# Performance work log

Measured on AMD Instinct MI355X. Metric: run time of the kernel, lower is better.

## Reference

```python
import jax, jax.numpy as jnp
import numpy as np

B, M, E, H = 256, 196, 1024, 8
Dh = E // H          # 128 = att_mid_dim[0]
MID = 64             # att_mid_dim[1]
ALPHA = 1.3          # CELU alpha
EPS = 1e-5


def group_norm(x, w, b, groups=H, eps=EPS):
    # x: [N, C]; torch GroupNorm over channel groups
    N, C = x.shape
    xg = x.reshape(N, groups, C // groups)
    mu = xg.mean(-1, keepdims=True)
    var = xg.var(-1, keepdims=True)
    xn = ((xg - mu) * jax.lax.rsqrt(var + eps)).reshape(N, C)
    return xn * w + b


def proj(x, W, b, gw, gb):
    # Linear -> CELU(1.3) -> GroupNorm(H)
    return group_norm(jax.nn.celu(x @ W + b, alpha=ALPHA), gw, gb)


def setup_inputs() -> dict:
    key0 = jax.random.key(0)
    ks = jax.random.split(key0, 16)
    d = {}
    d["query"] = jax.random.normal(ks[0], (B, E), jnp.float32)
    d["key"] = jax.random.normal(ks[1], (B, M, E), jnp.float32)
    d["mask"] = jax.random.randint(ks[2], (B, M), 0, 2, jnp.int32)
    d["value1"] = jax.random.normal(ks[3], (B, E), jnp.float32)
    d["value2"] = jax.random.normal(ks[4], (B, M, E), jnp.float32)
    s = 0.02
    for i, nm in enumerate(["q", "k", "v1", "v2"]):
        d[f"W{nm}"] = jax.random.normal(ks[5 + i], (E, E), jnp.float32) * s
        d[f"b{nm}"] = jnp.zeros((E,), jnp.float32)
        d[f"g{nm}_w"] = jnp.ones((E,), jnp.float32)
        d[f"g{nm}_b"] = jnp.zeros((E,), jnp.float32)
    d["Wb"] = jax.random.normal(ks[9], (Dh, MID), jnp.float32) * s
    d["bb"] = jnp.zeros((MID,), jnp.float32)
    d["Ws"] = jax.random.normal(ks[10], (MID, 1), jnp.float32) * s
    d["bs"] = jnp.zeros((1,), jnp.float32)
    d["Wc"] = jax.random.normal(ks[11], (MID, Dh), jnp.float32) * s
    d["bc"] = jnp.zeros((Dh,), jnp.float32)
    return d


def reference(query, key, mask, value1, value2,
              Wq, bq, gq_w, gq_b, Wk, bk, gk_w, gk_b,
              Wv1, bv1, gv1_w, gv1_b, Wv2, bv2, gv2_w, gv2_b,
              Wb, bb, Ws, bs, Wc, bc):
    # input projections (dropout layers are identity at eval)
    q = proj(query, Wq, bq, gq_w, gq_b).reshape(B, H, Dh)
    v1 = proj(value1, Wv1, bv1, gv1_w, gv1_b).reshape(B, H, Dh)
    k = proj(key.reshape(-1, E), Wk, bk, gk_w, gk_b).reshape(B, M, H, Dh).transpose(0, 2, 1, 3)   # [B,H,M,Dh]
    v2 = proj(value2.reshape(-1, E), Wv2, bv2, gv2_w, gv2_b).reshape(B, M, H, Dh).transpose(0, 2, 1, 3)

    # SCAttDec
    att_map = q[:, :, None, :] * k                                # [B,H,M,Dh]
    hidden = jax.nn.relu(att_map @ Wb + bb)                       # [B,H,M,MID]
    maskf = mask.astype(hidden.dtype)                             # [B,M]
    mext = maskf[:, None, :, None]                                # [B,1,M,1]
    att_map_pool = jnp.sum(hidden * mext, axis=2) / jnp.sum(mext, axis=2)   # [B,H,MID]

    alpha_spatial = (hidden @ Ws + bs)[..., 0]                    # [B,H,M]
    alpha_spatial = jnp.where(mask[:, None, :] == 0, -1e9, alpha_spatial)
    alpha_spatial = jax.nn.softmax(alpha_spatial, axis=-1)
    v2_pooled = jnp.einsum("bhm,bhmd->bhd", alpha_spatial, v2)    # [B,H,Dh]

    alpha_channel = jax.nn.sigmoid(att_map_pool @ Wc + bc)        # [B,H,Dh]
    attn = v1 * v2_pooled * alpha_channel                         # [B,H,Dh]
    return attn.reshape(B, H * Dh)
```

## Files before the change

### kernel.cpp

```cpp
#include <hip/hip_runtime.h>

typedef unsigned short u16;
typedef unsigned int u32;
typedef unsigned long long u64;
typedef __attribute__((ext_vector_type(8))) short short8;
typedef __attribute__((ext_vector_type(4))) float floatx4;

#define E_ 1024
#define B_ 256
#define M_ 196
#define H_ 8
#define DH_ 128
#define MID_ 64
#define NKROW 50176

__device__ __forceinline__ u16 f2bf(float f){
  union { float f; u32 u; } v; v.f = f;
  return (u16)((v.u + (((v.u >> 16) & 1u) + 0x7fffu)) >> 16);
}
__device__ __forceinline__ float bf2f(u16 h){
  union { u32 u; float f; } v; v.u = ((u32)h) << 16;
  return v.f;
}
__device__ __forceinline__ u32 pack_bf2(float a, float b){
  u32 ua = __float_as_uint(a) + 0x8000u;
  u32 ub = __float_as_uint(b) + 0x8000u;
  return __builtin_amdgcn_perm(ub, ua, 0x07060302);
}
__device__ __forceinline__ void gl_lds16(const void* g, void* l){
  __builtin_amdgcn_global_load_lds(
      (const __attribute__((address_space(1))) u32*)g,
      (__attribute__((address_space(3))) u32*)l, 16, 0, 0);
}
__device__ __forceinline__ float celu_f(float x){
  float xn = 1.3f * (__expf(x * 0.76923076923f) - 1.0f);
  return x > 0.f ? x : xn;
}

__global__ __launch_bounds__(256) void xconv_kernel(
    float* __restrict__ key, float* __restrict__ value2,
    float* __restrict__ query, float* __restrict__ value1)
{
  int gr = blockIdx.x * 8 + (threadIdx.x >> 5);
  int i  = threadIdx.x & 31;
  float* X; int r;
  if (gr < NKROW)               { X = key;    r = gr; }
  else if (gr < 2*NKROW)        { X = value2; r = gr - NKROW; }
  else if (gr < 2*NKROW + B_)   { X = query;  r = gr - 2*NKROW; }
  else                          { X = value1; r = gr - 2*NKROW - B_; }
  const float4* src = (const float4*)(X + (size_t)r * E_);
  float4 v[8];
  #pragma unroll
  for (int j = 0; j < 8; j++) v[j] = src[j * 32 + i];
  __syncthreads();
  uint2* dst = (uint2*)((u16*)X + (size_t)r * 2048);
  #pragma unroll
  for (int j = 0; j < 8; j++){
    uint2 o;
    o.x = pack_bf2(v[j].x, v[j].y);
    o.y = pack_bf2(v[j].z, v[j].w);
    dst[j * 32 + i] = o;
  }
}

__global__ __launch_bounds__(256) void wconv_kernel(
    const float* __restrict__ Wq, const float* __restrict__ Wk,
    const float* __restrict__ Wv1, const float* __restrict__ Wv2,
    u16* __restrict__ Wt)
{
  __shared__ u16 tile[64][72];
  const float* W = (blockIdx.z == 0) ? Wq : (blockIdx.z == 1) ? Wk
                 : (blockIdx.z == 2) ? Wv1 : Wv2;
  u16* out = Wt + (size_t)blockIdx.z * (E_ * E_);
  int k0 = blockIdx.x * 64, c0 = blockIdx.y * 64;
  int tx = threadIdx.x & 63, ty = threadIdx.x >> 6;
  #pragma unroll
  for (int i = 0; i < 16; i++){
    int k = ty * 16 + i;
    tile[k][tx] = f2bf(W[(size_t)(k0 + k) * E_ + c0 + tx]);
  }
  __syncthreads();
  #pragma unroll
  for (int i = 0; i < 16; i++){
    int c = ty * 16 + i;
    out[(size_t)(c0 + c) * E_ + k0 + tx] = tile[tx][c];
  }
}

__global__ __launch_bounds__(512, 2) void proj_kernel(
    const u16* __restrict__ xq_, const u16* __restrict__ xk_,
    const u16* __restrict__ xv1_, const u16* __restrict__ xv2_,
    const float* __restrict__ bq, const float* __restrict__ gqw, const float* __restrict__ gqb,
    const float* __restrict__ bk, const float* __restrict__ gkw, const float* __restrict__ gkb,
    const float* __restrict__ bv1, const float* __restrict__ gv1w, const float* __restrict__ gv1b,
    const float* __restrict__ bv2, const float* __restrict__ gv2w, const float* __restrict__ gv2b,
    const u16* __restrict__ Wt,
    u16* __restrict__ qout, u16* __restrict__ khead,
    u16* __restrict__ v1out, u16* __restrict__ v2head)
{
  __shared__ __align__(16) u16 a_lds[2][256 * 32];
  __shared__ __align__(16) u16 b_lds[2][256 * 32];

  const int tid = threadIdx.x;
  const int w = tid >> 6, lane = tid & 63, qd = lane >> 4, lr = lane & 15;
  const int wm = w & 3, wn = w >> 2;

  const int mtb = blockIdx.x;
  const u16* X; const float *bias, *gw, *gb; u16* outp; int row0, matsel, hm;
  if (mtb < 196)      { X = xk_;  bias = bk;  gw = gkw;  gb = gkb;  outp = khead;  row0 = mtb*256;        matsel = 1; hm = 1; }
  else if (mtb < 392) { X = xv2_; bias = bv2; gw = gv2w; gb = gv2b; outp = v2head; row0 = (mtb-196)*256;  matsel = 3; hm = 1; }
  else if (mtb == 392){ X = xq_;  bias = bq;  gw = gqw;  gb = gqb;  outp = qout;   row0 = 0;              matsel = 0; hm = 0; }
  else                { X = xv1_; bias = bv1; gw = gv1w; gb = gv1b; outp = v1out;  row0 = 0;              matsel = 2; hm = 0; }
  const int cp = blockIdx.y, col0 = cp * 256;

  const int srow = lane >> 2, sslot = lane & 3, sswz = sslot ^ (srow & 3);
  const u16* aptr0 = X + (size_t)(row0 + (w*2    )*16 + srow) * 2048 + sswz * 8;
  const u16* aptr1 = X + (size_t)(row0 + (w*2 + 1)*16 + srow) * 2048 + sswz * 8;
  const u16* wbase = Wt + (size_t)matsel * (E_*E_);
  const u16* bptr0 = wbase + (size_t)(col0 + (w*2    )*16 + srow) * E_ + sswz * 8;
  const u16* bptr1 = wbase + (size_t)(col0 + (w*2 + 1)*16 + srow) * E_ + sswz * 8;

  floatx4 acc[4][8];
  #pragma unroll
  for (int i = 0; i < 4; i++)
    #pragma unroll
    for (int j = 0; j < 8; j++){
      floatx4 z = {0.f, 0.f, 0.f, 0.f};
      acc[i][j] = z;
    }

  gl_lds16(aptr0, &a_lds[0][(w*2    )*16*32]);
  gl_lds16(aptr1, &a_lds[0][(w*2 + 1)*16*32]);
  gl_lds16(bptr0, &b_lds[0][(w*2    )*16*32]);
  gl_lds16(bptr1, &b_lds[0][(w*2 + 1)*16*32]);
  __syncthreads();

  const int fslot = (qd ^ (lr & 3)) * 8;
  for (int kt = 0; kt < 32; kt++){
    const int cur = kt & 1, nxt = cur ^ 1;
    if (kt < 31){
      const int ko = (kt + 1) * 32;
      gl_lds16(aptr0 + ko, &a_lds[nxt][(w*2    )*16*32]);
      gl_lds16(aptr1 + ko, &a_lds[nxt][(w*2 + 1)*16*32]);
      gl_lds16(bptr0 + ko, &b_lds[nxt][(w*2    )*16*32]);
      gl_lds16(bptr1 + ko, &b_lds[nxt][(w*2 + 1)*16*32]);
    }
    short8 afr[4], bfr[8];
    #pragma unroll
    for (int m2 = 0; m2 < 4; m2++)
      afr[m2] = *(const short8*)&a_lds[cur][(wm*64 + m2*16 + lr)*32 + fslot];
    #pragma unroll
    for (int nt = 0; nt < 8; nt++)
      bfr[nt] = *(const short8*)&b_lds[cur][(wn*128 + nt*16 + lr)*32 + fslot];
    #pragma unroll
    for (int m2 = 0; m2 < 4; m2++)
      #pragma unroll
      for (int nt = 0; nt < 8; nt++)
        acc[m2][nt] = __builtin_amdgcn_mfma_f32_16x16x32_bf16(afr[m2], bfr[nt], acc[m2][nt], 0, 0, 0);
    __syncthreads();
  }

  float biasv[8], gwv[8], gbv[8];
  #pragma unroll
  for (int nt = 0; nt < 8; nt++){
    int c = col0 + wn*128 + nt*16 + lr;
    biasv[nt] = bias[c]; gwv[nt] = gw[c]; gbv[nt] = gb[c];
  }
  const int head = cp*2 + wn;
  #pragma unroll
  for (int m2 = 0; m2 < 4; m2++){
    #pragma unroll
    for (int r = 0; r < 4; r++){
      float s = 0.f, s2 = 0.f;
      #pragma unroll
      for (int nt = 0; nt < 8; nt++){
        float x = celu_f(acc[m2][nt][r] + biasv[nt]);
        acc[m2][nt][r] = x;
        s += x; s2 += x * x;
      }
      #pragma unroll
      for (int off = 1; off < 16; off <<= 1){
        s  += __shfl_xor(s,  off, 64);
        s2 += __shfl_xor(s2, off, 64);
      }
      float mean = s * 0.0078125f;
      float var  = s2 * 0.0078125f - mean * mean;
      float rstd = rsqrtf(var + 1e-5f);
      u32 rg = row0 + wm*64 + m2*16 + qd*4 + r;
      size_t base;
      if (hm){
        u32 bi = (u32)(((u64)rg * 171197ull) >> 25);
        u32 m  = rg - bi * 196u;
        base = ((size_t)(bi*H_ + head)*M_ + m) * DH_;
      } else {
        base = (size_t)rg * E_ + head * DH_;
      }
      #pragma unroll
      for (int nt = 0; nt < 8; nt++)
        outp[base + nt*16 + lr] = f2bf((acc[m2][nt][r] - mean) * rstd * gwv[nt] + gbv[nt]);
    }
  }
}

__global__ __launch_bounds__(256) void attn_kernel(
    const u16* __restrict__ qproj, const u16* __restrict__ khead,
    const u16* __restrict__ v1proj, const u16* __restrict__ v2head,
    const int* __restrict__ mask,
    const float* __restrict__ Wb, const float* __restrict__ bb,
    const float* __restrict__ Ws, const float* __restrict__ bs,
    const float* __restrict__ Wc, const float* __restrict__ bc,
    float* __restrict__ outp)
{
  __shared__ u16 wbt[64 * 136];
  __shared__ float qv[128];
  __shared__ float mrow[208];
  __shared__ float logitv[208];
  __shared__ float hsum_l[4][64];
  __shared__ float wexpv[208];
  __shared__ float poolv[64];
  __shared__ float v2acc[4][128];
  __shared__ float wc2[2][128];
  __shared__ float red[8];

  const int tid = threadIdx.x;
  const int w = tid >> 6, lane = tid & 63, qd = lane >> 4, lr = lane & 15;
  const int b = blockIdx.y, h = blockIdx.x;

  const u16* kbase  = khead  + (size_t)(b*H_ + h) * (M_*DH_);
  const u16* v2base = v2head + (size_t)(b*H_ + h) * (M_*DH_);

  if (tid < 128) qv[tid] = bf2f(qproj[(size_t)b * E_ + h * DH_ + tid]);
  if (tid < 208) mrow[tid] = (tid < M_) ? (float)mask[b * M_ + tid] : 0.f;
  __syncthreads();

  {
    int n = tid & 63, kb = (tid >> 6) * 32;
    #pragma unroll
    for (int kk = 0; kk < 32; kk++)
      wbt[n * 136 + kb + kk] = f2bf(qv[kb + kk] * Wb[(kb + kk) * MID_ + n]);
  }
  __syncthreads();

  float wsv[4], bbv[4];
  #pragma unroll
  for (int nt = 0; nt < 4; nt++){ wsv[nt] = Ws[nt * 16 + lr]; bbv[nt] = bb[nt * 16 + lr]; }
  const float bsv = bs[0];
  float hs[4] = {0, 0, 0, 0};

  for (int mt = w; mt < 13; mt += 4){
    int mrow_g = mt * 16 + lr;
    int mcl = (mrow_g < M_) ? mrow_g : (M_ - 1);
    const u16* arow = kbase + (size_t)mcl * DH_;
    floatx4 hacc[4];
    #pragma unroll
    for (int nt = 0; nt < 4; nt++){ floatx4 z = {0.f, 0.f, 0.f, 0.f}; hacc[nt] = z; }
    #pragma unroll
    for (int kc = 0; kc < 4; kc++){
      short8 afr = *(const short8*)(arow + kc * 32 + qd * 8);
      #pragma unroll
      for (int nt = 0; nt < 4; nt++){
        short8 bfr = *(const short8*)&wbt[(nt * 16 + lr) * 136 + kc * 32 + qd * 8];
        hacc[nt] = __builtin_amdgcn_mfma_f32_16x16x32_bf16(afr, bfr, hacc[nt], 0, 0, 0);
      }
    }
    float lp[4] = {0, 0, 0, 0};
    #pragma unroll
    for (int nt = 0; nt < 4; nt++){
      #pragma unroll
      for (int r = 0; r < 4; r++){
        float hv = hacc[nt][r] + bbv[nt];
        hv = fmaxf(hv, 0.f);
        lp[r] += hv * wsv[nt];
        hs[nt] += mrow[mt * 16 + qd * 4 + r] * hv;
      }
    }
    #pragma unroll
    for (int r = 0; r < 4; r++){
      float a = lp[r];
      #pragma unroll
      for (int off = 1; off < 16; off <<= 1) a += __shfl_xor(a, off, 64);
      if (lr == 0) logitv[mt * 16 + qd * 4 + r] = a + bsv;
    }
  }
  #pragma unroll
  for (int nt = 0; nt < 4; nt++){
    hs[nt] += __shfl_xor(hs[nt], 16, 64);
    hs[nt] += __shfl_xor(hs[nt], 32, 64);
  }
  if (lane < 16){
    #pragma unroll
    for (int nt = 0; nt < 4; nt++) hsum_l[w][nt * 16 + lane] = hs[nt];
  }
  __syncthreads();

  if (w == 0){
    float s = 0.f;
    for (int m = lane; m < M_; m += 64) s += mrow[m];
    #pragma unroll
    for (int off = 1; off < 64; off <<= 1) s += __shfl_xor(s, off, 64);
    if (lane == 0) red[0] = s;
  } else if (w == 1){
    float mx = -1e30f;
    for (int m = lane; m < M_; m += 64) if (mrow[m] > 0.5f) mx = fmaxf(mx, logitv[m]);
    #pragma unroll
    for (int off = 1; off < 64; off <<= 1) mx = fmaxf(mx, __shfl_xor(mx, off, 64));
    if (lane == 0) red[1] = mx;
  } else if (w == 2){
    poolv[lane & 63] = hsum_l[0][lane & 63] + hsum_l[1][lane & 63]
                     + hsum_l[2][lane & 63] + hsum_l[3][lane & 63];
  }
  __syncthreads();
  const float cnt = red[0], mx = red[1];
  if (tid < 208)
    wexpv[tid] = (tid < M_ && mrow[tid] > 0.5f) ? __expf(logitv[tid] - mx) : 0.f;
  __syncthreads();
  if (w == 0){
    float s = 0.f;
    for (int m = lane; m < M_; m += 64) s += wexpv[m];
    #pragma unroll
    for (int off = 1; off < 64; off <<= 1) s += __shfl_xor(s, off, 64);
    if (lane == 0) red[2] = s;
  } else if (w == 1){
    poolv[lane & 63] = poolv[lane & 63] / cnt;
  }
  __syncthreads();
  const float S = red[2];

  {
    float ac[8] = {0, 0, 0, 0, 0, 0, 0, 0};
    #pragma unroll
    for (int it = 0; it < 13; it++){
      int m = it * 16 + w * 4 + qd;
      if (m < M_){
        float we = wexpv[m];
        uint4 u = *(const uint4*)(v2base + (size_t)m * DH_ + lr * 8);
        ac[0] += we * bf2f((u16)(u.x & 0xffff));
        ac[1] += we * bf2f((u16)(u.x >> 16));
        ac[2] += we * bf2f((u16)(u.y & 0xffff));
        ac[3] += we * bf2f((u16)(u.y >> 16));
        ac[4] += we * bf2f((u16)(u.z & 0xffff));
        ac[5] += we * bf2f((u16)(u.z >> 16));
        ac[6] += we * bf2f((u16)(u.w & 0xffff));
        ac[7] += we * bf2f((u16)(u.w >> 16));
      }
    }
    #pragma unroll
    for (int j = 0; j < 8; j++){
      ac[j] += __shfl_xor(ac[j], 16, 64);
      ac[j] += __shfl_xor(ac[j], 32, 64);
    }
    if (qd == 0){
      #pragma unroll
      for (int j = 0; j < 8; j++) v2acc[w][lr * 8 + j] = ac[j];
    }
  }
  __syncthreads();

  {
    int d = tid & 127, jh = tid >> 7;
    float a = 0.f;
    #pragma unroll 8
    for (int j = jh * 32; j < jh * 32 + 32; j++) a += poolv[j] * Wc[j * DH_ + d];
    wc2[jh][d] = a;
  }
  __syncthreads();

  if (tid < 128){
    float a = wc2[0][tid] + wc2[1][tid];
    float acv = 1.f / (1.f + __expf(-(a + bc[tid])));
    float vp = (v2acc[0][tid] + v2acc[1][tid] + v2acc[2][tid] + v2acc[3][tid]) / S;
    float o = bf2f(v1proj[(size_t)b * E_ + h * DH_ + tid]) * vp * acv;
    outp[(size_t)b * E_ + h * DH_ + tid] = o;
  }
}

extern "C" void kernel_launch(void* const* d_in, const int* in_sizes, int n_in,
                              void* d_out, int out_size, void* d_ws, size_t ws_size,
                              hipStream_t stream)
{
  float* query  = (float*)d_in[0];
  float* key    = (float*)d_in[1];
  const int* mask = (const int*)d_in[2];
  float* value1 = (float*)d_in[3];
  float* value2 = (float*)d_in[4];
  const float* Wq  = (const float*)d_in[5];
  const float* bq  = (const float*)d_in[6];
  const float* gqw = (const float*)d_in[7];
  const float* gqb = (const float*)d_in[8];
  const float* Wk  = (const float*)d_in[9];
  const float* bk  = (const float*)d_in[10];
  const float* gkw = (const float*)d_in[11];
  const float* gkb = (const float*)d_in[12];
  const float* Wv1 = (const float*)d_in[13];
  const float* bv1 = (const float*)d_in[14];
  const float* gv1w= (const float*)d_in[15];
  const float* gv1b= (const float*)d_in[16];
  const float* Wv2 = (const float*)d_in[17];
  const float* bv2 = (const float*)d_in[18];
  const float* gv2w= (const float*)d_in[19];
  const float* gv2b= (const float*)d_in[20];
  const float* Wb  = (const float*)d_in[21];
  const float* bb  = (const float*)d_in[22];
  const float* Ws  = (const float*)d_in[23];
  const float* bs  = (const float*)d_in[24];
  const float* Wc  = (const float*)d_in[25];
  const float* bc  = (const float*)d_in[26];

  const size_t NHD = (size_t)B_ * H_ * M_ * DH_;
  u16* khead  = (u16*)d_ws;
  u16* v2head = khead  + NHD;
  u16* qout   = v2head + NHD;
  u16* v1out  = qout   + (size_t)B_ * E_;
  u16* Wt     = v1out  + (size_t)B_ * E_;

  xconv_kernel<<<(2*NKROW + 2*B_)/8, 256, 0, stream>>>(key, value2, query, value1);

  dim3 g0(16, 16, 4);
  wconv_kernel<<<g0, 256, 0, stream>>>(Wq, Wk, Wv1, Wv2, Wt);

  dim3 g1(394, 4);
  proj_kernel<<<g1, 512, 0, stream>>>(
      (const u16*)query, (const u16*)key, (const u16*)value1, (const u16*)value2,
      bq, gqw, gqb, bk, gkw, gkb, bv1, gv1w, gv1b, bv2, gv2w, gv2b,
      Wt, qout, khead, v1out, v2head);

  dim3 g2(H_, B_);
  attn_kernel<<<g2, 256, 0, stream>>>(qout, khead, v1out, v2head, mask,
      Wb, bb, Ws, bs, Wc, bc, (float*)d_out);
}
```

Baseline: 924.0 us.

## Drop LDS staging in projection GEMM and prefetch v2 rows in attention

The projection GEMM no longer stages tiles through double-buffered LDS. It now uses 128x128 tiles per 256-thread block, one head per block, and each wave loads its A and B MFMA fragments straight from global memory. This removes the LDS traffic and the per-iteration barriers, but it gives up operand reuse: all four waves fetch the same B fragments and rely on cache hits. In the attention kernel, the v2 rows are loaded into registers before the softmax reductions so their latency overlaps with that work. One barrier that was not needed is also removed.

```diff
diff --git a/kernel.cpp b/kernel.cpp
--- a/kernel.cpp
+++ b/kernel.cpp
@@ -26,11 +26,6 @@
   u32 ua = __float_as_uint(a) + 0x8000u;
   u32 ub = __float_as_uint(b) + 0x8000u;
   return __builtin_amdgcn_perm(ub, ua, 0x07060302);
-}
-__device__ __forceinline__ void gl_lds16(const void* g, void* l){
-  __builtin_amdgcn_global_load_lds(
-      (const __attribute__((address_space(1))) u32*)g,
-      (__attribute__((address_space(3))) u32*)l, 16, 0, 0);
 }
 __device__ __forceinline__ float celu_f(float x){
   float xn = 1.3f * (__expf(x * 0.76923076923f) - 1.0f);
@@ -87,7 +82,7 @@
   }
 }
 
-__global__ __launch_bounds__(512, 2) void proj_kernel(
+__global__ __launch_bounds__(256) void proj_kernel(
     const u16* __restrict__ xq_, const u16* __restrict__ xk_,
     const u16* __restrict__ xv1_, const u16* __restrict__ xv2_,
     const float* __restrict__ bq, const float* __restrict__ gqw, const float* __restrict__ gqb,
@@ -98,77 +93,55 @@
     u16* __restrict__ qout, u16* __restrict__ khead,
     u16* __restrict__ v1out, u16* __restrict__ v2head)
 {
-  __shared__ __align__(16) u16 a_lds[2][256 * 32];
-  __shared__ __align__(16) u16 b_lds[2][256 * 32];
-
   const int tid = threadIdx.x;
   const int w = tid >> 6, lane = tid & 63, qd = lane >> 4, lr = lane & 15;
-  const int wm = w & 3, wn = w >> 2;
 
   const int mtb = blockIdx.x;
   const u16* X; const float *bias, *gw, *gb; u16* outp; int row0, matsel, hm;
-  if (mtb < 196)      { X = xk_;  bias = bk;  gw = gkw;  gb = gkb;  outp = khead;  row0 = mtb*256;        matsel = 1; hm = 1; }
-  else if (mtb < 392) { X = xv2_; bias = bv2; gw = gv2w; gb = gv2b; outp = v2head; row0 = (mtb-196)*256;  matsel = 3; hm = 1; }
-  else if (mtb == 392){ X = xq_;  bias = bq;  gw = gqw;  gb = gqb;  outp = qout;   row0 = 0;              matsel = 0; hm = 0; }
-  else                { X = xv1_; bias = bv1; gw = gv1w; gb = gv1b; outp = v1out;  row0 = 0;              matsel = 2; hm = 0; }
-  const int cp = blockIdx.y, col0 = cp * 256;
-
-  const int srow = lane >> 2, sslot = lane & 3, sswz = sslot ^ (srow & 3);
-  const u16* aptr0 = X + (size_t)(row0 + (w*2    )*16 + srow) * 2048 + sswz * 8;
-  const u16* aptr1 = X + (size_t)(row0 + (w*2 + 1)*16 + srow) * 2048 + sswz * 8;
+  if (mtb < 392)      { X = xk_;  bias = bk;  gw = gkw;  gb = gkb;  outp = khead;  row0 = mtb*128;        matsel = 1; hm = 1; }
+  else if (mtb < 784) { X = xv2_; bias = bv2; gw = gv2w; gb = gv2b; outp = v2head; row0 = (mtb-392)*128;  matsel = 3; hm = 1; }
+  else if (mtb < 786) { X = xq_;  bias = bq;  gw = gqw;  gb = gqb;  outp = qout;   row0 = (mtb-784)*128;  matsel = 0; hm = 0; }
+  else                { X = xv1_; bias = bv1; gw = gv1w; gb = gv1b; outp = v1out;  row0 = (mtb-786)*128;  matsel = 2; hm = 0; }
+  const int head = blockIdx.y, col0 = head * DH_;
+
+  const u16* ap0 = X + (size_t)(row0 + w*32 + lr) * 2048 + qd * 8;
+  const u16* ap1 = ap0 + (size_t)16 * 2048;
   const u16* wbase = Wt + (size_t)matsel * (E_*E_);
-  const u16* bptr0 = wbase + (size_t)(col0 + (w*2    )*16 + srow) * E_ + sswz * 8;
-  const u16* bptr1 = wbase + (size_t)(col0 + (w*2 + 1)*16 + srow) * E_ + sswz * 8;
-
-  floatx4 acc[4][8];
-  #pragma unroll
-  for (int i = 0; i < 4; i++)
+  const u16* bp = wbase + (size_t)(col0 + lr) * E_ + qd * 8;
+
+  floatx4 acc[2][8];
+  #pragma unroll
+  for (int i = 0; i < 2; i++)
     #pragma unroll
     for (int j = 0; j < 8; j++){
       floatx4 z = {0.f, 0.f, 0.f, 0.f};
       acc[i][j] = z;
     }
 
-  gl_lds16(aptr0, &a_lds[0][(w*2    )*16*32]);
-  gl_lds16(aptr1, &a_lds[0][(w*2 + 1)*16*32]);
-  gl_lds16(bptr0, &b_lds[0][(w*2    )*16*32]);
-  gl_lds16(bptr1, &b_lds[0][(w*2 + 1)*16*32]);
-  __syncthreads();
-
-  const int fslot = (qd ^ (lr & 3)) * 8;
+  #pragma unroll 2
   for (int kt = 0; kt < 32; kt++){
-    const int cur = kt & 1, nxt = cur ^ 1;
-    if (kt < 31){
-      const int ko = (kt + 1) * 32;
-      gl_lds16(aptr0 + ko, &a_lds[nxt][(w*2    )*16*32]);
-      gl_lds16(aptr1 + ko, &a_lds[nxt][(w*2 + 1)*16*32]);
-      gl_lds16(bptr0 + ko, &b_lds[nxt][(w*2    )*16*32]);
-      gl_lds16(bptr1 + ko, &b_lds[nxt][(w*2 + 1)*16*32]);
-    }
-    short8 afr[4], bfr[8];
-    #pragma unroll
-    for (int m2 = 0; m2 < 4; m2++)
-      afr[m2] = *(const short8*)&a_lds[cur][(wm*64 + m2*16 + lr)*32 + fslot];
+    const int ko = kt * 32;
+    short8 a0 = *(const short8*)(ap0 + ko);
+    short8 a1 = *(const short8*)(ap1 + ko);
+    short8 bf[8];
     #pragma unroll
     for (int nt = 0; nt < 8; nt++)
-      bfr[nt] = *(const short8*)&b_lds[cur][(wn*128 + nt*16 + lr)*32 + fslot];
-    #pragma unroll
-    for (int m2 = 0; m2 < 4; m2++)
-      #pragma unroll
-      for (int nt = 0; nt < 8; nt++)
-        acc[m2][nt] = __builtin_amdgcn_mfma_f32_16x16x32_bf16(afr[m2], bfr[nt], acc[m2][nt], 0, 0, 0);
-    __syncthreads();
+      bf[nt] = *(const short8*)(bp + (size_t)nt * 16 * E_ + ko);
+    #pragma unroll
+    for (int nt = 0; nt < 8; nt++){
+      acc[0][nt] = __builtin_amdgcn_mfma_f32_16x16x32_bf16(a0, bf[nt], acc[0][nt], 0, 0, 0);
+      acc[1][nt] = __builtin_amdgcn_mfma_f32_16x16x32_bf16(a1, bf[nt], acc[1][nt], 0, 0, 0);
+    }
   }
 
   float biasv[8], gwv[8], gbv[8];
   #pragma unroll
   for (int nt = 0; nt < 8; nt++){
-    int c = col0 + wn*128 + nt*16 + lr;
+    int c = col0 + nt*16 + lr;
     biasv[nt] = bias[c]; gwv[nt] = gw[c]; gbv[nt] = gb[c];
   }
-  const int head = cp*2 + wn;
-  #pragma unroll
-  for (int m2 = 0; m2 < 4; m2++){
+  #pragma unroll
+  for (int m2 = 0; m2 < 2; m2++){
     #pragma unroll
     for (int r = 0; r < 4; r++){
       float s = 0.f, s2 = 0.f;
@@ -186,7 +159,7 @@
       float mean = s * 0.0078125f;
       float var  = s2 * 0.0078125f - mean * mean;
       float rstd = rsqrtf(var + 1e-5f);
-      u32 rg = row0 + wm*64 + m2*16 + qd*4 + r;
+      u32 rg = row0 + w*32 + m2*16 + qd*4 + r;
       size_t base;
       if (hm){
         u32 bi = (u32)(((u64)rg * 171197ull) >> 25);
@@ -247,7 +220,10 @@
   const float bsv = bs[0];
   float hs[4] = {0, 0, 0, 0};
 
-  for (int mt = w; mt < 13; mt += 4){
+  #pragma unroll
+  for (int it = 0; it < 4; it++){
+    int mt = w + it * 4;
+    if (mt >= 13) continue;
     int mrow_g = mt * 16 + lr;
     int mcl = (mrow_g < M_) ? mrow_g : (M_ - 1);
     const u16* arow = kbase + (size_t)mcl * DH_;
@@ -291,6 +267,14 @@
     #pragma unroll
     for (int nt = 0; nt < 4; nt++) hsum_l[w][nt * 16 + lane] = hs[nt];
   }
+
+  uint4 v2r[13];
+  #pragma unroll
+  for (int it = 0; it < 13; it++){
+    int m = it * 16 + w * 4 + qd;
+    int msafe = (m < M_) ? m : 0;
+    v2r[it] = *(const uint4*)(v2base + (size_t)msafe * DH_ + lr * 8);
+  }
   __syncthreads();
 
   if (w == 0){
@@ -331,18 +315,16 @@
     #pragma unroll
     for (int it = 0; it < 13; it++){
       int m = it * 16 + w * 4 + qd;
-      if (m < M_){
-        float we = wexpv[m];
-        uint4 u = *(const uint4*)(v2base + (size_t)m * DH_ + lr * 8);
-        ac[0] += we * bf2f((u16)(u.x & 0xffff));
-        ac[1] += we * bf2f((u16)(u.x >> 16));
-        ac[2] += we * bf2f((u16)(u.y & 0xffff));
-        ac[3] += we * bf2f((u16)(u.y >> 16));
-        ac[4] += we * bf2f((u16)(u.z & 0xffff));
-        ac[5] += we * bf2f((u16)(u.z >> 16));
-        ac[6] += we * bf2f((u16)(u.w & 0xffff));
-        ac[7] += we * bf2f((u16)(u.w >> 16));
-      }
+      float we = (m < M_) ? wexpv[m] : 0.f;
+      uint4 u = v2r[it];
+      ac[0] += we * bf2f((u16)(u.x & 0xffff));
+      ac[1] += we * bf2f((u16)(u.x >> 16));
+      ac[2] += we * bf2f((u16)(u.y & 0xffff));
+      ac[3] += we * bf2f((u16)(u.y >> 16));
+      ac[4] += we * bf2f((u16)(u.z & 0xffff));
+      ac[5] += we * bf2f((u16)(u.z >> 16));
+      ac[6] += we * bf2f((u16)(u.w & 0xffff));
+      ac[7] += we * bf2f((u16)(u.w >> 16));
     }
     #pragma unroll
     for (int j = 0; j < 8; j++){
@@ -354,7 +336,6 @@
       for (int j = 0; j < 8; j++) v2acc[w][lr * 8 + j] = ac[j];
     }
   }
-  __syncthreads();
 
   {
     int d = tid & 127, jh = tid >> 7;
@@ -418,8 +399,8 @@
   dim3 g0(16, 16, 4);
   wconv_kernel<<<g0, 256, 0, stream>>>(Wq, Wk, Wv1, Wv2, Wt);
 
-  dim3 g1(394, 4);
-  proj_kernel<<<g1, 512, 0, stream>>>(
+  dim3 g1(788, 8);
+  proj_kernel<<<g1, 256, 0, stream>>>(
       (const u16*)query, (const u16*)key, (const u16*)value1, (const u16*)value2,
       bq, gqw, gqb, bk, gkw, gkb, bv1, gv1w, gv1b, bv2, gv2w, gv2b,
       Wt, qout, khead, v1out, v2head);
```

New measurement: 1.436 ms. +55.4%, slower.
